# Performance work log

Hardware: AMD Instinct MI355X
Metric: run time of the kernel (lower is better)

Reference implementation:

```python
import jax, jax.numpy as jnp
import numpy as np

N, E, IN_DIM, HID, HEADS, OUT_DIM, N_GRAPHS = 50000, 640000, 128, 64, 8, 2, 64
NEG_SLOPE = 0.2  # PyG GATConv default leaky_relu slope


def setup_inputs() -> dict:
    key = jax.random.key(0)
    ks = jax.random.split(key, 12)
    x = jax.random.normal(ks[0], (N, IN_DIM), jnp.float32)
    edge_index = jax.random.randint(ks[1], (2, E), 0, N, jnp.int32)
    batch = jnp.sort(jax.random.randint(ks[2], (N,), 0, N_GRAPHS, jnp.int32))
    def glorot(k, shape):
        fan_in = shape[0]
        return jax.random.normal(k, shape, jnp.float32) / np.sqrt(fan_in)
    return {
        "x": x,
        "W1": glorot(ks[3], (IN_DIM, HEADS * HID)),
        "att_src1": glorot(ks[4], (HEADS, HID)),
        "att_dst1": glorot(ks[5], (HEADS, HID)),
        "b1": jnp.zeros((HEADS * HID,), jnp.float32),
        "W2": glorot(ks[6], (HEADS * HID, HID)),
        "att_src2": glorot(ks[7], (1, HID)),
        "att_dst2": glorot(ks[8], (1, HID)),
        "b2": jnp.zeros((HID,), jnp.float32),
        "fc_w": glorot(ks[9], (HID, OUT_DIM)),
        "fc_b": jnp.zeros((OUT_DIM,), jnp.float32),
        "edge_index": edge_index,
        "batch": batch,
    }


def gat_layer(x, src, dst, W, a_src, a_dst, bias):
    # PyG GATConv: h = x @ W per head; alpha_e = LeakyReLU(a_src.h_src + a_dst.h_dst),
    # softmax over edges sharing the same dst, weighted scatter-sum, concat heads.
    H, C = a_src.shape
    h = (x @ W).reshape(-1, H, C)                       # [N, H, C]
    a_s = jnp.einsum('nhc,hc->nh', h, a_src)            # [N, H]
    a_d = jnp.einsum('nhc,hc->nh', h, a_dst)
    e = jax.nn.leaky_relu(a_s[src] + a_d[dst], NEG_SLOPE)  # [Etot, H]
    e_max = jax.ops.segment_max(e, dst, num_segments=N)
    e = jnp.exp(e - e_max[dst])
    denom = jax.ops.segment_sum(e, dst, num_segments=N)
    alpha = e / (denom[dst] + 1e-16)                    # edge softmax
    msg = h[src] * alpha[..., None]                     # [Etot, H, C]
    out = jax.ops.segment_sum(msg, dst, num_segments=N) # [N, H, C]
    return out.reshape(-1, H * C) + bias


def reference(x, W1, att_src1, att_dst1, b1, W2, att_src2, att_dst2, b2, fc_w, fc_b, edge_index, batch):
    # add self-loops (PyG GATConv default add_self_loops=True)
    loop = jnp.arange(N, dtype=edge_index.dtype)
    src = jnp.concatenate([edge_index[0], loop])
    dst = jnp.concatenate([edge_index[1], loop])

    h = gat_layer(x, src, dst, W1, att_src1, att_dst1, b1)   # [N, HEADS*HID]
    h = jax.nn.elu(h)
    # dropout is identity at eval
    h = gat_layer(h, src, dst, W2, att_src2, att_dst2, b2)   # [N, HID]
    h = jax.nn.elu(h)

    # global mean pool over graphs
    sums = jax.ops.segment_sum(h, batch, num_segments=N_GRAPHS)
    cnts = jax.ops.segment_sum(jnp.ones((N, 1), h.dtype), batch, num_segments=N_GRAPHS)
    pooled = sums / jnp.maximum(cnts, 1.0)                   # [G, HID]
    return pooled @ fc_w + fc_b                              # [G, OUT_DIM]
```

## Files before the change

kernel.cpp:

```cpp
#include <hip/hip_runtime.h>
#include <hip/hip_bf16.h>
#include <cstdint>
#include <cstddef>

#define N_NODES   50000
#define N_EDGES   640000
#define ETOT      (N_EDGES + N_NODES)
#define IN_DIM    128
#define HID       64
#define HEADS     8
#define F1        (HEADS * HID)
#define OUT_DIM   2
#define N_GRAPHS  64
#define NEG_SLOPE 0.2f
#define CAP       64

typedef __attribute__((ext_vector_type(8))) short s8v;
typedef __attribute__((ext_vector_type(4))) float f32x4;
typedef __attribute__((ext_vector_type(2))) float f32x2;
typedef unsigned char uchar;
typedef unsigned int  uint;

__device__ __forceinline__ float leakyf(float x) { return x > 0.f ? x : NEG_SLOPE * x; }
__device__ __forceinline__ float eluf(float x)   { return x > 0.f ? x : __expf(x) - 1.f; }

__device__ __forceinline__ float bf2f(ushort u) {
    union { uint32_t i; float f; } c; c.i = ((uint32_t)u) << 16; return c.f;
}
__device__ __forceinline__ ushort f2bf(float f) {
    union { float f; uint32_t i; } c; c.f = f;
    uint32_t r = c.i + 0x7FFFu + ((c.i >> 16) & 1u);
    return (ushort)(r >> 16);
}
template<int SEL>
__device__ __forceinline__ float fp8f(uint w) {
    return __builtin_amdgcn_cvt_f32_fp8(w, SEL);
}
template<bool HI>
__device__ __forceinline__ f32x2 pk8(uint w) {
    return __builtin_amdgcn_cvt_pk_f32_fp8(w, HI);
}
__device__ __forceinline__ uchar f2fp8(float f) {
    uint p = __builtin_amdgcn_cvt_pk_fp8_f32(f, f, 0u, false);
    return (uchar)(p & 0xFFu);
}

#define XW_ITEMS  (N_NODES * IN_DIM / 4)
#define W1_ITEMS  (F1 * IN_DIM)
#define W2_ITEMS  (HID * F1)
#define PREP_ITEMS (ETOT + XW_ITEMS + W1_ITEMS + W2_ITEMS)

__global__ __launch_bounds__(256) void prep_fill(const int* __restrict__ srcI,
                                                 const int* __restrict__ dstI,
                                                 int* __restrict__ counts,
                                                 ushort* __restrict__ csrp,
                                                 const float* __restrict__ x,
                                                 const float* __restrict__ W1,
                                                 const float* __restrict__ W2,
                                                 ushort* __restrict__ xb,
                                                 ushort* __restrict__ W1T,
                                                 ushort* __restrict__ W2T) {
    int i = blockIdx.x * 256 + threadIdx.x;
    if (i < ETOT) {
        int s, d;
        if (i < N_EDGES) { s = srcI[i]; d = dstI[i]; }
        else             { s = d = i - N_EDGES; }
        int slot = atomicAdd(&counts[d], 1);
        if (slot < CAP) csrp[d * CAP + slot] = (ushort)s;
    } else if (i < ETOT + XW_ITEMS) {
        int idx = i - ETOT;
        float4 v = *reinterpret_cast<const float4*>(x + (size_t)idx * 4);
        ushort4 u;
        u.x = f2bf(v.x); u.y = f2bf(v.y); u.z = f2bf(v.z); u.w = f2bf(v.w);
        *reinterpret_cast<ushort4*>(xb + (size_t)idx * 4) = u;
    } else if (i < ETOT + XW_ITEMS + W1_ITEMS) {
        int idx = i - ETOT - XW_ITEMS;
        int n = idx >> 7, k = idx & 127;
        W1T[idx] = f2bf(W1[(size_t)k * F1 + n]);
    } else if (i < PREP_ITEMS) {
        int idx = i - ETOT - XW_ITEMS - W1_ITEMS;
        int n = idx >> 9, k = idx & 511;
        W2T[idx] = f2bf(W2[(size_t)k * HID + n]);
    }
}

template<int BM, int BN, int BK, int AH>
__global__ __launch_bounds__(256) void gemm_att(const ushort* __restrict__ A,
                                                const ushort* __restrict__ BT,
                                                uchar* __restrict__ C8,
                                                int M, int N, int K,
                                                const float* __restrict__ att_s,
                                                const float* __restrict__ att_d,
                                                float* __restrict__ as_o,
                                                float* __restrict__ ad_o) {
    int nwg = gridDim.x;
    int q = nwg >> 3, r = nwg & 7;
    int xcd = blockIdx.x & 7, loc = blockIdx.x >> 3;
    int sid = (xcd < r) ? (xcd * (q + 1) + loc)
                        : (r * (q + 1) + (xcd - r) * q + loc);
    int ncb = N / BN;
    int bx = sid % ncb;
    int by = sid / ncb;

    __shared__ ushort As[BM * BK];
    __shared__ ushort Bs[BN * BK];
    const int t    = threadIdx.x;
    const int row0 = by * BM;
    const int col0 = bx * BN;
    const int lane = t & 63;
    const int wr   = t >> 6;
    constexpr int FR = BM / 64;

    f32x4 acc[FR][4];
    #pragma unroll
    for (int i = 0; i < FR; ++i)
        #pragma unroll
        for (int j = 0; j < 4; ++j)
            acc[i][j] = (f32x4){0.f, 0.f, 0.f, 0.f};

    constexpr int A_IT = BM * BK / 8 / 256;
    constexpr int B_IT = BN * BK / 8 / 256;

    for (int k0 = 0; k0 < K; k0 += BK) {
        #pragma unroll
        for (int i = 0; i < A_IT; ++i) {
            int ch  = t + 256 * i;
            int rr  = ch >> 3;
            int c16 = ch & 7;
            uint4 v = make_uint4(0u, 0u, 0u, 0u);
            int gr = row0 + rr;
            if (gr < M)
                v = *reinterpret_cast<const uint4*>(A + (size_t)gr * K + k0 + c16 * 8);
            int off = (ch * 16) ^ ((rr & 7) << 4);
            *reinterpret_cast<uint4*>(reinterpret_cast<char*>(As) + off) = v;
        }
        #pragma unroll
        for (int i = 0; i < B_IT; ++i) {
            int ch  = t + 256 * i;
            int rr  = ch >> 3;
            int c16 = ch & 7;
            uint4 v = *reinterpret_cast<const uint4*>(BT + (size_t)(col0 + rr) * K + k0 + c16 * 8);
            int off = (ch * 16) ^ ((rr & 7) << 4);
            *reinterpret_cast<uint4*>(reinterpret_cast<char*>(Bs) + off) = v;
        }
        __syncthreads();
        #pragma unroll
        for (int kk = 0; kk < BK; kk += 32) {
            s8v af[FR], bf[4];
            #pragma unroll
            for (int fr = 0; fr < FR; ++fr) {
                int rr  = wr * (FR * 16) + fr * 16 + (lane & 15);
                int off = (rr * (BK * 2) + kk * 2 + (lane >> 4) * 16) ^ ((rr & 7) << 4);
                af[fr] = *reinterpret_cast<const s8v*>(reinterpret_cast<const char*>(As) + off);
            }
            #pragma unroll
            for (int fc = 0; fc < 4; ++fc) {
                int rr  = fc * 16 + (lane & 15);
                int off = (rr * (BK * 2) + kk * 2 + (lane >> 4) * 16) ^ ((rr & 7) << 4);
                bf[fc] = *reinterpret_cast<const s8v*>(reinterpret_cast<const char*>(Bs) + off);
            }
            #pragma unroll
            for (int fr = 0; fr < FR; ++fr)
                #pragma unroll
                for (int fc = 0; fc < 4; ++fc)
                    acc[fr][fc] = __builtin_amdgcn_mfma_f32_16x16x32_bf16(af[fr], bf[fc], acc[fr][fc], 0, 0, 0);
        }
        __syncthreads();
    }

    float avs[4], avd[4];
    const float* asp = att_s + bx * BN;
    const float* adp = att_d + bx * BN;
    #pragma unroll
    for (int fc = 0; fc < 4; ++fc) {
        avs[fc] = asp[fc * 16 + (lane & 15)];
        avd[fc] = adp[fc * 16 + (lane & 15)];
    }

    #pragma unroll
    for (int fr = 0; fr < FR; ++fr) {
        #pragma unroll
        for (int j = 0; j < 4; ++j) {
            int row = row0 + wr * (FR * 16) + fr * 16 + (lane >> 4) * 4 + j;
            if (row < M) {
                float sv = 0.f, dv = 0.f;
                #pragma unroll
                for (int fc = 0; fc < 4; ++fc) {
                    float c = acc[fr][fc][j];
                    int col = col0 + fc * 16 + (lane & 15);
                    C8[(size_t)row * N + col] = f2fp8(c);
                    sv = fmaf(c, avs[fc], sv);
                    dv = fmaf(c, avd[fc], dv);
                }
                #pragma unroll
                for (int off = 1; off < 16; off <<= 1) {
                    sv += __shfl_xor(sv, off);
                    dv += __shfl_xor(dv, off);
                }
                if ((lane & 15) == 0) {
                    as_o[(size_t)row * AH + bx] = sv;
                    ad_o[(size_t)row * AH + bx] = dv;
                }
            }
        }
    }
}

__global__ __launch_bounds__(256) void gat_agg1(const uchar* __restrict__ h8,
                                                const float* __restrict__ as,
                                                const float* __restrict__ ad,
                                                const int* __restrict__ counts,
                                                const ushort* __restrict__ csrp,
                                                const float* __restrict__ bias,
                                                ushort* __restrict__ z) {
    __shared__ float lds_w[4][HEADS][CAP + 1];
    int tid  = threadIdx.x;
    int wid  = tid >> 6;
    int dst  = (blockIdx.x * 256 + tid) >> 6;
    int lane = tid & 63;
    if (dst >= N_NODES) return;
    int cnt = min(counts[dst], CAP);
    int hd  = lane >> 3;

    int myidx = (lane < cnt) ? (int)csrp[(size_t)dst * CAP + lane] : 0;
    float4 a0 = *reinterpret_cast<const float4*>(as + (size_t)myidx * HEADS);
    float4 a1 = *reinterpret_cast<const float4*>(as + (size_t)myidx * HEADS + 4);
    float4 d0 = *reinterpret_cast<const float4*>(ad + (size_t)dst * HEADS);
    float4 d1 = *reinterpret_cast<const float4*>(ad + (size_t)dst * HEADS + 4);
    lds_w[wid][0][lane] = __expf(leakyf(a0.x + d0.x));
    lds_w[wid][1][lane] = __expf(leakyf(a0.y + d0.y));
    lds_w[wid][2][lane] = __expf(leakyf(a0.z + d0.z));
    lds_w[wid][3][lane] = __expf(leakyf(a0.w + d0.w));
    lds_w[wid][4][lane] = __expf(leakyf(a1.x + d1.x));
    lds_w[wid][5][lane] = __expf(leakyf(a1.y + d1.y));
    lds_w[wid][6][lane] = __expf(leakyf(a1.z + d1.z));
    lds_w[wid][7][lane] = __expf(leakyf(a1.w + d1.w));

    f32x2 acc2[4];
    acc2[0] = (f32x2){0.f, 0.f}; acc2[1] = (f32x2){0.f, 0.f};
    acc2[2] = (f32x2){0.f, 0.f}; acc2[3] = (f32x2){0.f, 0.f};
    float den = 0.f;
    const uchar* hb = h8 + (size_t)lane * 8;
    for (int j0 = 0; j0 < cnt; j0 += 4) {
        int n = cnt - j0;
        int s0 = 0, s1 = 0, s2 = 0, s3 = 0;
        uint2 v0 = {}, v1 = {}, v2 = {}, v3 = {};
        float w0 = 0.f, w1 = 0.f, w2 = 0.f, w3 = 0.f;
        s0 = __shfl(myidx, j0);
        v0 = *reinterpret_cast<const uint2*>(hb + (size_t)s0 * F1);
        w0 = lds_w[wid][hd][j0];
        if (n > 1) {
            s1 = __shfl(myidx, j0 + 1);
            v1 = *reinterpret_cast<const uint2*>(hb + (size_t)s1 * F1);
            w1 = lds_w[wid][hd][j0 + 1];
        }
        if (n > 2) {
            s2 = __shfl(myidx, j0 + 2);
            v2 = *reinterpret_cast<const uint2*>(hb + (size_t)s2 * F1);
            w2 = lds_w[wid][hd][j0 + 2];
        }
        if (n > 3) {
            s3 = __shfl(myidx, j0 + 3);
            v3 = *reinterpret_cast<const uint2*>(hb + (size_t)s3 * F1);
            w3 = lds_w[wid][hd][j0 + 3];
        }
        {
            f32x2 wv = (f32x2){w0, w0};
            den += w0;
            acc2[0] += pk8<false>(v0.x) * wv;
            acc2[1] += pk8<true >(v0.x) * wv;
            acc2[2] += pk8<false>(v0.y) * wv;
            acc2[3] += pk8<true >(v0.y) * wv;
        }
        if (n > 1) {
            f32x2 wv = (f32x2){w1, w1};
            den += w1;
            acc2[0] += pk8<false>(v1.x) * wv;
            acc2[1] += pk8<true >(v1.x) * wv;
            acc2[2] += pk8<false>(v1.y) * wv;
            acc2[3] += pk8<true >(v1.y) * wv;
        }
        if (n > 2) {
            f32x2 wv = (f32x2){w2, w2};
            den += w2;
            acc2[0] += pk8<false>(v2.x) * wv;
            acc2[1] += pk8<true >(v2.x) * wv;
            acc2[2] += pk8<false>(v2.y) * wv;
            acc2[3] += pk8<true >(v2.y) * wv;
        }
        if (n > 3) {
            f32x2 wv = (f32x2){w3, w3};
            den += w3;
            acc2[0] += pk8<false>(v3.x) * wv;
            acc2[1] += pk8<true >(v3.x) * wv;
            acc2[2] += pk8<false>(v3.y) * wv;
            acc2[3] += pk8<true >(v3.y) * wv;
        }
    }
    float inv = 1.f / (den + 1e-16f);
    s8v ov;
    #pragma unroll
    for (int c = 0; c < 8; ++c) {
        float v = acc2[c >> 1][c & 1] * inv + bias[lane * 8 + c];
        ov[c] = (short)f2bf(eluf(v));
    }
    *reinterpret_cast<s8v*>(z + (size_t)dst * F1 + lane * 8) = ov;
}

__global__ __launch_bounds__(256) void gat_agg2(const uchar* __restrict__ h8,
                                                const float* __restrict__ as,
                                                const float* __restrict__ ad,
                                                const int* __restrict__ counts,
                                                const ushort* __restrict__ csrp,
                                                const float* __restrict__ bias,
                                                float* __restrict__ z) {
    int dst  = (blockIdx.x * 256 + threadIdx.x) >> 6;
    int lane = threadIdx.x & 63;
    if (dst >= N_NODES) return;
    int cnt = min(counts[dst], CAP);
    float adv = ad[dst];

    int myidx = (lane < cnt) ? (int)csrp[(size_t)dst * CAP + lane] : 0;
    float wl  = (lane < cnt) ? __expf(leakyf(as[myidx] + adv)) : 0.f;
    float den = wl;
    #pragma unroll
    for (int off = 32; off > 0; off >>= 1) den += __shfl_xor(den, off);

    float acc = 0.f;
    for (int j0 = 0; j0 < cnt; j0 += 4) {
        int n = cnt - j0;
        int s0 = 0, s1 = 0, s2 = 0, s3 = 0;
        float w0 = 0.f, w1 = 0.f, w2 = 0.f, w3 = 0.f;
        uint b0 = 0, b1 = 0, b2 = 0, b3 = 0;
        s0 = __shfl(myidx, j0);     w0 = __shfl(wl, j0);
        b0 = h8[(size_t)s0 * HID + lane];
        if (n > 1) { s1 = __shfl(myidx, j0 + 1); w1 = __shfl(wl, j0 + 1); b1 = h8[(size_t)s1 * HID + lane]; }
        if (n > 2) { s2 = __shfl(myidx, j0 + 2); w2 = __shfl(wl, j0 + 2); b2 = h8[(size_t)s2 * HID + lane]; }
        if (n > 3) { s3 = __shfl(myidx, j0 + 3); w3 = __shfl(wl, j0 + 3); b3 = h8[(size_t)s3 * HID + lane]; }
        acc = fmaf(w0, fp8f<0>(b0), acc);
        if (n > 1) acc = fmaf(w1, fp8f<0>(b1), acc);
        if (n > 2) acc = fmaf(w2, fp8f<0>(b2), acc);
        if (n > 3) acc = fmaf(w3, fp8f<0>(b3), acc);
    }
    float v = acc / (den + 1e-16f) + bias[lane];
    z[(size_t)dst * HID + lane] = eluf(v);
}

__global__ __launch_bounds__(512) void pool_fc(const float* __restrict__ z,
                                               const int* __restrict__ batch,
                                               const float* __restrict__ fc_w,
                                               const float* __restrict__ fc_b,
                                               float* __restrict__ out) {
    int g = blockIdx.x;
    int t = threadIdx.x, lane = t & 63, w = t >> 6;
    auto lb = [&](int key) {
        int lo = 0, hi = N_NODES;
        while (lo < hi) { int mid = (lo + hi) >> 1; if (batch[mid] < key) lo = mid + 1; else hi = mid; }
        return lo;
    };
    int lo = lb(g), hi = lb(g + 1);
    float a0 = 0.f, a1 = 0.f, a2 = 0.f, a3 = 0.f;
    for (int n0 = lo + (w << 2); n0 < hi; n0 += 32) {
        a0 += z[(size_t)n0 * HID + lane];
        if (n0 + 1 < hi) a1 += z[(size_t)(n0 + 1) * HID + lane];
        if (n0 + 2 < hi) a2 += z[(size_t)(n0 + 2) * HID + lane];
        if (n0 + 3 < hi) a3 += z[(size_t)(n0 + 3) * HID + lane];
    }
    float acc = (a0 + a1) + (a2 + a3);
    __shared__ float sh[8][HID];
    sh[w][lane] = acc;
    __syncthreads();
    if (w == 0) {
        float s = 0.f;
        #pragma unroll
        for (int i = 0; i < 8; ++i) s += sh[i][lane];
        float cntf = fmaxf((float)(hi - lo), 1.f);
        float mean = s / cntf;
        float p0 = mean * fc_w[lane * OUT_DIM + 0];
        float p1 = mean * fc_w[lane * OUT_DIM + 1];
        #pragma unroll
        for (int off = 32; off > 0; off >>= 1) {
            p0 += __shfl_xor(p0, off);
            p1 += __shfl_xor(p1, off);
        }
        if (lane == 0) {
            out[g * OUT_DIM + 0] = p0 + fc_b[0];
            out[g * OUT_DIM + 1] = p1 + fc_b[1];
        }
    }
}

extern "C" void kernel_launch(void* const* d_in, const int* in_sizes, int n_in,
                              void* d_out, int out_size, void* d_ws, size_t ws_size,
                              hipStream_t stream) {
    const float* x    = (const float*)d_in[0];
    const float* W1   = (const float*)d_in[1];
    const float* at_s1= (const float*)d_in[2];
    const float* at_d1= (const float*)d_in[3];
    const float* b1   = (const float*)d_in[4];
    const float* W2   = (const float*)d_in[5];
    const float* at_s2= (const float*)d_in[6];
    const float* at_d2= (const float*)d_in[7];
    const float* b2   = (const float*)d_in[8];
    const float* fcw  = (const float*)d_in[9];
    const float* fcb  = (const float*)d_in[10];
    const int*   ei   = (const int*)d_in[11];
    const int*   batch= (const int*)d_in[12];
    float* out = (float*)d_out;

    char* p = (char*)d_ws;
    auto alloc = [&](size_t bytes) {
        char* r = p;
        p += (bytes + 255) & ~size_t(255);
        return r;
    };
    int*    counts= (int*)alloc((size_t)N_NODES * 4);
    ushort* xb    = (ushort*)alloc((size_t)N_NODES * IN_DIM * 2);
    ushort* W1T   = (ushort*)alloc((size_t)F1 * IN_DIM * 2);
    ushort* W2T   = (ushort*)alloc((size_t)HID * F1 * 2);
    uchar*  h1    = (uchar*)alloc((size_t)N_NODES * F1);
    ushort* z1    = (ushort*)alloc((size_t)N_NODES * F1 * 2);
    uchar*  h2    = (uchar*)alloc((size_t)N_NODES * HID);
    float*  z2    = (float*)alloc((size_t)N_NODES * HID * 4);
    float*  as1   = (float*)alloc((size_t)N_NODES * HEADS * 4);
    float*  ad1   = (float*)alloc((size_t)N_NODES * HEADS * 4);
    float*  as2   = (float*)alloc((size_t)N_NODES * 4);
    float*  ad2   = (float*)alloc((size_t)N_NODES * 4);
    ushort* csrp  = (ushort*)alloc((size_t)N_NODES * CAP * 2);

    const int* srcI = ei;
    const int* dstI = ei + N_EDGES;

    (void)hipMemsetAsync(counts, 0, (size_t)N_NODES * 4, stream);

    prep_fill<<<(PREP_ITEMS + 255) / 256, 256, 0, stream>>>(
        srcI, dstI, counts, csrp, x, W1, W2, xb, W1T, W2T);

    int nwg1 = (F1 / 64) * ((N_NODES + 127) / 128);
    gemm_att<128, 64, 64, HEADS><<<nwg1, 256, 0, stream>>>(
        xb, W1T, h1, N_NODES, F1, IN_DIM, at_s1, at_d1, as1, ad1);
    gat_agg1<<<(N_NODES + 3) / 4, 256, 0, stream>>>(h1, as1, ad1, counts, csrp, b1, z1);

    int nwg2 = 1 * ((N_NODES + 63) / 64);
    gemm_att<64, 64, 64, 1><<<nwg2, 256, 0, stream>>>(
        z1, W2T, h2, N_NODES, HID, F1, at_s2, at_d2, as2, ad2);
    gat_agg2<<<(N_NODES + 3) / 4, 256, 0, stream>>>(h2, as2, ad2, counts, csrp, b2, z2);

    pool_fc<<<N_GRAPHS, 512, 0, stream>>>(z2, batch, fcw, fcb, out);
}
```

Before: 285.4 us.

## Fuse x bf16 conversion into GEMM, pack fp8 stores with permuted column layout

Measured after the change: 308.5 us. 8.1% more time.

```diff
diff --git a/kernel.cpp b/kernel.cpp
--- a/kernel.cpp
+++ b/kernel.cpp
@@ -20,13 +20,11 @@
 typedef __attribute__((ext_vector_type(2))) float f32x2;
 typedef unsigned char uchar;
 typedef unsigned int  uint;
+typedef unsigned long long u64;
 
 __device__ __forceinline__ float leakyf(float x) { return x > 0.f ? x : NEG_SLOPE * x; }
 __device__ __forceinline__ float eluf(float x)   { return x > 0.f ? x : __expf(x) - 1.f; }
 
-__device__ __forceinline__ float bf2f(ushort u) {
-    union { uint32_t i; float f; } c; c.i = ((uint32_t)u) << 16; return c.f;
-}
 __device__ __forceinline__ ushort f2bf(float f) {
     union { float f; uint32_t i; } c; c.f = f;
     uint32_t r = c.i + 0x7FFFu + ((c.i >> 16) & 1u);
@@ -40,26 +38,27 @@
 __device__ __forceinline__ f32x2 pk8(uint w) {
     return __builtin_amdgcn_cvt_pk_f32_fp8(w, HI);
 }
-__device__ __forceinline__ uchar f2fp8(float f) {
-    uint p = __builtin_amdgcn_cvt_pk_fp8_f32(f, f, 0u, false);
-    return (uchar)(p & 0xFFu);
-}
-
-#define XW_ITEMS  (N_NODES * IN_DIM / 4)
+__device__ __forceinline__ int orig64(int q) { return ((q & 3) << 4) | (q >> 2); }
+
 #define W1_ITEMS  (F1 * IN_DIM)
 #define W2_ITEMS  (HID * F1)
-#define PREP_ITEMS (ETOT + XW_ITEMS + W1_ITEMS + W2_ITEMS)
+#define PM_ITEMS  (F1 + HID + HID * OUT_DIM)
+#define PREP_ITEMS (ETOT + W1_ITEMS + W2_ITEMS + PM_ITEMS)
 
 __global__ __launch_bounds__(256) void prep_fill(const int* __restrict__ srcI,
                                                  const int* __restrict__ dstI,
                                                  int* __restrict__ counts,
                                                  ushort* __restrict__ csrp,
-                                                 const float* __restrict__ x,
                                                  const float* __restrict__ W1,
                                                  const float* __restrict__ W2,
-                                                 ushort* __restrict__ xb,
+                                                 const float* __restrict__ b1,
+                                                 const float* __restrict__ b2,
+                                                 const float* __restrict__ fcw,
                                                  ushort* __restrict__ W1T,
-                                                 ushort* __restrict__ W2T) {
+                                                 ushort* __restrict__ W2T,
+                                                 float* __restrict__ b1p,
+                                                 float* __restrict__ b2p,
+                                                 float* __restrict__ fcwp) {
     int i = blockIdx.x * 256 + threadIdx.x;
     if (i < ETOT) {
         int s, d;
@@ -67,25 +66,32 @@
         else             { s = d = i - N_EDGES; }
         int slot = atomicAdd(&counts[d], 1);
         if (slot < CAP) csrp[d * CAP + slot] = (ushort)s;
-    } else if (i < ETOT + XW_ITEMS) {
+    } else if (i < ETOT + W1_ITEMS) {
         int idx = i - ETOT;
-        float4 v = *reinterpret_cast<const float4*>(x + (size_t)idx * 4);
-        ushort4 u;
-        u.x = f2bf(v.x); u.y = f2bf(v.y); u.z = f2bf(v.z); u.w = f2bf(v.w);
-        *reinterpret_cast<ushort4*>(xb + (size_t)idx * 4) = u;
-    } else if (i < ETOT + XW_ITEMS + W1_ITEMS) {
-        int idx = i - ETOT - XW_ITEMS;
         int n = idx >> 7, k = idx & 127;
         W1T[idx] = f2bf(W1[(size_t)k * F1 + n]);
+    } else if (i < ETOT + W1_ITEMS + W2_ITEMS) {
+        int idx = i - ETOT - W1_ITEMS;
+        int n = idx >> 9, kp = idx & 511;
+        int ko = (kp & 448) | orig64(kp & 63);
+        W2T[idx] = f2bf(W2[(size_t)ko * HID + n]);
     } else if (i < PREP_ITEMS) {
-        int idx = i - ETOT - XW_ITEMS - W1_ITEMS;
-        int n = idx >> 9, k = idx & 511;
-        W2T[idx] = f2bf(W2[(size_t)k * HID + n]);
-    }
-}
-
-template<int BM, int BN, int BK, int AH>
-__global__ __launch_bounds__(256) void gemm_att(const ushort* __restrict__ A,
+        int j = i - ETOT - W1_ITEMS - W2_ITEMS;
+        if (j < F1) {
+            b1p[j] = b1[(j & ~63) | orig64(j & 63)];
+        } else if (j < F1 + HID) {
+            int q = j - F1;
+            b2p[q] = b2[orig64(q)];
+        } else {
+            int q = j - F1 - HID;
+            int ch = q >> 1, o = q & 1;
+            fcwp[q] = fcw[orig64(ch) * OUT_DIM + o];
+        }
+    }
+}
+
+template<int BM, int BN, int BK, int AH, bool AF32>
+__global__ __launch_bounds__(256) void gemm_att(const void* __restrict__ Av,
                                                 const ushort* __restrict__ BT,
                                                 uchar* __restrict__ C8,
                                                 int M, int N, int K,
@@ -127,10 +133,24 @@
             int ch  = t + 256 * i;
             int rr  = ch >> 3;
             int c16 = ch & 7;
+            int gr = row0 + rr;
             uint4 v = make_uint4(0u, 0u, 0u, 0u);
-            int gr = row0 + rr;
-            if (gr < M)
-                v = *reinterpret_cast<const uint4*>(A + (size_t)gr * K + k0 + c16 * 8);
+            if constexpr (AF32) {
+                const float* Af = (const float*)Av;
+                if (gr < M) {
+                    const float* pr = Af + (size_t)gr * K + k0 + c16 * 8;
+                    float4 f0 = *reinterpret_cast<const float4*>(pr);
+                    float4 f1 = *reinterpret_cast<const float4*>(pr + 4);
+                    v.x = ((uint)f2bf(f0.y) << 16) | f2bf(f0.x);
+                    v.y = ((uint)f2bf(f0.w) << 16) | f2bf(f0.z);
+                    v.z = ((uint)f2bf(f1.y) << 16) | f2bf(f1.x);
+                    v.w = ((uint)f2bf(f1.w) << 16) | f2bf(f1.z);
+                }
+            } else {
+                const ushort* Ab = (const ushort*)Av;
+                if (gr < M)
+                    v = *reinterpret_cast<const uint4*>(Ab + (size_t)gr * K + k0 + c16 * 8);
+            }
             int off = (ch * 16) ^ ((rr & 7) << 4);
             *reinterpret_cast<uint4*>(reinterpret_cast<char*>(As) + off) = v;
         }
@@ -183,12 +203,13 @@
         for (int j = 0; j < 4; ++j) {
             int row = row0 + wr * (FR * 16) + fr * 16 + (lane >> 4) * 4 + j;
             if (row < M) {
+                uint pk = __builtin_amdgcn_cvt_pk_fp8_f32(acc[fr][0][j], acc[fr][1][j], 0u, false);
+                pk = __builtin_amdgcn_cvt_pk_fp8_f32(acc[fr][2][j], acc[fr][3][j], pk, true);
+                *reinterpret_cast<uint*>(C8 + (size_t)row * N + col0 + (lane & 15) * 4) = pk;
                 float sv = 0.f, dv = 0.f;
                 #pragma unroll
                 for (int fc = 0; fc < 4; ++fc) {
                     float c = acc[fr][fc][j];
-                    int col = col0 + fc * 16 + (lane & 15);
-                    C8[(size_t)row * N + col] = f2fp8(c);
                     sv = fmaf(c, avs[fc], sv);
                     dv = fmaf(c, avd[fc], dv);
                 }
@@ -211,7 +232,7 @@
                                                 const float* __restrict__ ad,
                                                 const int* __restrict__ counts,
                                                 const ushort* __restrict__ csrp,
-                                                const float* __restrict__ bias,
+                                                const float* __restrict__ b1p,
                                                 ushort* __restrict__ z) {
     __shared__ float lds_w[4][HEADS][CAP + 1];
     int tid  = threadIdx.x;
@@ -244,64 +265,64 @@
     for (int j0 = 0; j0 < cnt; j0 += 4) {
         int n = cnt - j0;
         int s0 = 0, s1 = 0, s2 = 0, s3 = 0;
-        uint2 v0 = {}, v1 = {}, v2 = {}, v3 = {};
+        u64 v0 = 0, v1 = 0, v2 = 0, v3 = 0;
         float w0 = 0.f, w1 = 0.f, w2 = 0.f, w3 = 0.f;
         s0 = __shfl(myidx, j0);
-        v0 = *reinterpret_cast<const uint2*>(hb + (size_t)s0 * F1);
+        v0 = __builtin_nontemporal_load(reinterpret_cast<const u64*>(hb + (size_t)s0 * F1));
         w0 = lds_w[wid][hd][j0];
         if (n > 1) {
             s1 = __shfl(myidx, j0 + 1);
-            v1 = *reinterpret_cast<const uint2*>(hb + (size_t)s1 * F1);
+            v1 = __builtin_nontemporal_load(reinterpret_cast<const u64*>(hb + (size_t)s1 * F1));
             w1 = lds_w[wid][hd][j0 + 1];
         }
         if (n > 2) {
             s2 = __shfl(myidx, j0 + 2);
-            v2 = *reinterpret_cast<const uint2*>(hb + (size_t)s2 * F1);
+            v2 = __builtin_nontemporal_load(reinterpret_cast<const u64*>(hb + (size_t)s2 * F1));
             w2 = lds_w[wid][hd][j0 + 2];
         }
         if (n > 3) {
             s3 = __shfl(myidx, j0 + 3);
-            v3 = *reinterpret_cast<const uint2*>(hb + (size_t)s3 * F1);
+            v3 = __builtin_nontemporal_load(reinterpret_cast<const u64*>(hb + (size_t)s3 * F1));
             w3 = lds_w[wid][hd][j0 + 3];
         }
         {
             f32x2 wv = (f32x2){w0, w0};
             den += w0;
-            acc2[0] += pk8<false>(v0.x) * wv;
-            acc2[1] += pk8<true >(v0.x) * wv;
-            acc2[2] += pk8<false>(v0.y) * wv;
-            acc2[3] += pk8<true >(v0.y) * wv;
+            acc2[0] += pk8<false>((uint)v0) * wv;
+            acc2[1] += pk8<true >((uint)v0) * wv;
+            acc2[2] += pk8<false>((uint)(v0 >> 32)) * wv;
+            acc2[3] += pk8<true >((uint)(v0 >> 32)) * wv;
         }
         if (n > 1) {
             f32x2 wv = (f32x2){w1, w1};
             den += w1;
-            acc2[0] += pk8<false>(v1.x) * wv;
-            acc2[1] += pk8<true >(v1.x) * wv;
-            acc2[2] += pk8<false>(v1.y) * wv;
-            acc2[3] += pk8<true >(v1.y) * wv;
+            acc2[0] += pk8<false>((uint)v1) * wv;
+            acc2[1] += pk8<true >((uint)v1) * wv;
+            acc2[2] += pk8<false>((uint)(v1 >> 32)) * wv;
+            acc2[3] += pk8<true >((uint)(v1 >> 32)) * wv;
         }
         if (n > 2) {
             f32x2 wv = (f32x2){w2, w2};
             den += w2;
-            acc2[0] += pk8<false>(v2.x) * wv;
-            acc2[1] += pk8<true >(v2.x) * wv;
-            acc2[2] += pk8<false>(v2.y) * wv;
-            acc2[3] += pk8<true >(v2.y) * wv;
+            acc2[0] += pk8<false>((uint)v2) * wv;
+            acc2[1] += pk8<true >((uint)v2) * wv;
+            acc2[2] += pk8<false>((uint)(v2 >> 32)) * wv;
+            acc2[3] += pk8<true >((uint)(v2 >> 32)) * wv;
         }
         if (n > 3) {
             f32x2 wv = (f32x2){w3, w3};
             den += w3;
-            acc2[0] += pk8<false>(v3.x) * wv;
-            acc2[1] += pk8<true >(v3.x) * wv;
-            acc2[2] += pk8<false>(v3.y) * wv;
-            acc2[3] += pk8<true >(v3.y) * wv;
+            acc2[0] += pk8<false>((uint)v3) * wv;
+            acc2[1] += pk8<true >((uint)v3) * wv;
+            acc2[2] += pk8<false>((uint)(v3 >> 32)) * wv;
+            acc2[3] += pk8<true >((uint)(v3 >> 32)) * wv;
         }
     }
     float inv = 1.f / (den + 1e-16f);
     s8v ov;
     #pragma unroll
     for (int c = 0; c < 8; ++c) {
-        float v = acc2[c >> 1][c & 1] * inv + bias[lane * 8 + c];
+        float v = acc2[c >> 1][c & 1] * inv + b1p[lane * 8 + c];
         ov[c] = (short)f2bf(eluf(v));
     }
     *reinterpret_cast<s8v*>(z + (size_t)dst * F1 + lane * 8) = ov;
@@ -312,7 +333,7 @@
                                                 const float* __restrict__ ad,
                                                 const int* __restrict__ counts,
                                                 const ushort* __restrict__ csrp,
-                                                const float* __restrict__ bias,
+                                                const float* __restrict__ b2p,
                                                 float* __restrict__ z) {
     int dst  = (blockIdx.x * 256 + threadIdx.x) >> 6;
     int lane = threadIdx.x & 63;
@@ -342,13 +363,13 @@
         if (n > 2) acc = fmaf(w2, fp8f<0>(b2), acc);
         if (n > 3) acc = fmaf(w3, fp8f<0>(b3), acc);
     }
-    float v = acc / (den + 1e-16f) + bias[lane];
+    float v = acc / (den + 1e-16f) + b2p[lane];
     z[(size_t)dst * HID + lane] = eluf(v);
 }
 
 __global__ __launch_bounds__(512) void pool_fc(const float* __restrict__ z,
                                                const int* __restrict__ batch,
-                                               const float* __restrict__ fc_w,
+                                               const float* __restrict__ fcwp,
                                                const float* __restrict__ fc_b,
                                                float* __restrict__ out) {
     int g = blockIdx.x;
@@ -376,8 +397,8 @@
         for (int i = 0; i < 8; ++i) s += sh[i][lane];
         float cntf = fmaxf((float)(hi - lo), 1.f);
         float mean = s / cntf;
-        float p0 = mean * fc_w[lane * OUT_DIM + 0];
-        float p1 = mean * fc_w[lane * OUT_DIM + 1];
+        float p0 = mean * fcwp[lane * OUT_DIM + 0];
+        float p1 = mean * fcwp[lane * OUT_DIM + 1];
         #pragma unroll
         for (int off = 32; off > 0; off >>= 1) {
             p0 += __shfl_xor(p0, off);
@@ -415,9 +436,11 @@
         return r;
     };
     int*    counts= (int*)alloc((size_t)N_NODES * 4);
-    ushort* xb    = (ushort*)alloc((size_t)N_NODES * IN_DIM * 2);
     ushort* W1T   = (ushort*)alloc((size_t)F1 * IN_DIM * 2);
     ushort* W2T   = (ushort*)alloc((size_t)HID * F1 * 2);
+    float*  b1p   = (float*)alloc((size_t)F1 * 4);
+    float*  b2p   = (float*)alloc((size_t)HID * 4);
+    float*  fcwp  = (float*)alloc((size_t)HID * OUT_DIM * 4);
     uchar*  h1    = (uchar*)alloc((size_t)N_NODES * F1);
     ushort* z1    = (ushort*)alloc((size_t)N_NODES * F1 * 2);
     uchar*  h2    = (uchar*)alloc((size_t)N_NODES * HID);
@@ -434,17 +457,17 @@
     (void)hipMemsetAsync(counts, 0, (size_t)N_NODES * 4, stream);
 
     prep_fill<<<(PREP_ITEMS + 255) / 256, 256, 0, stream>>>(
-        srcI, dstI, counts, csrp, x, W1, W2, xb, W1T, W2T);
+        srcI, dstI, counts, csrp, W1, W2, b1, b2, fcw, W1T, W2T, b1p, b2p, fcwp);
 
     int nwg1 = (F1 / 64) * ((N_NODES + 127) / 128);
-    gemm_att<128, 64, 64, HEADS><<<nwg1, 256, 0, stream>>>(
-        xb, W1T, h1, N_NODES, F1, IN_DIM, at_s1, at_d1, as1, ad1);
-    gat_agg1<<<(N_NODES + 3) / 4, 256, 0, stream>>>(h1, as1, ad1, counts, csrp, b1, z1);
-
-    int nwg2 = 1 * ((N_NODES + 63) / 64);
-    gemm_att<64, 64, 64, 1><<<nwg2, 256, 0, stream>>>(
+    gemm_att<128, 64, 64, HEADS, true><<<nwg1, 256, 0, stream>>>(
+        x, W1T, h1, N_NODES, F1, IN_DIM, at_s1, at_d1, as1, ad1);
+    gat_agg1<<<(N_NODES + 3) / 4, 256, 0, stream>>>(h1, as1, ad1, counts, csrp, b1p, z1);
+
+    int nwg2 = 1 * ((N_NODES + 127) / 128);
+    gemm_att<128, 64, 64, 1, false><<<nwg2, 256, 0, stream>>>(
         z1, W2T, h2, N_NODES, HID, F1, at_s2, at_d2, as2, ad2);
-    gat_agg2<<<(N_NODES + 3) / 4, 256, 0, stream>>>(h2, as2, ad2, counts, csrp, b2, z2);
-
-    pool_fc<<<N_GRAPHS, 512, 0, stream>>>(z2, batch, fcw, fcb, out);
-}
+    gat_agg2<<<(N_NODES + 3) / 4, 256, 0, stream>>>(h2, as2, ad2, counts, csrp, b2p, z2);
+
+    pool_fc<<<N_GRAPHS, 512, 0, stream>>>(z2, batch, fcwp, fcb, out);
+}
```
